# Performance work log

Hardware: AMD Instinct MI355X
Metric: run time of the kernel (lower is better)

## Reference

```python
import jax, jax.numpy as jnp
import numpy as np

B, N, NODE_IN, RAW_IN, COV, H = 4096, 128, 16, 128, 8, 64
BN_EPS = 1e-5


def setup_inputs() -> dict:
    key = jax.random.key(0)
    ks = jax.random.split(key, 24)
    rn = lambda k, s, sc=0.1: jax.random.normal(k, s, jnp.float32) * sc
    return {
        'x_str': jax.random.normal(ks[0], (B, N, NODE_IN), jnp.float32),
        'x_raw': jax.random.normal(ks[1], (B, RAW_IN), jnp.float32),
        'adj': jax.random.uniform(ks[2], (B, N, N), jnp.float32),
        'x_cov': jax.random.normal(ks[3], (B, COV), jnp.float32),
        'age': jax.random.uniform(ks[4], (B, 1), jnp.float32),
        'gc1_w': rn(ks[5], (NODE_IN, H)), 'gc1_b': jnp.zeros((H,), jnp.float32),
        'gc2_w': rn(ks[6], (H, H)), 'gc2_b': jnp.zeros((H,), jnp.float32),
        'bn_gamma': jnp.ones((N,), jnp.float32), 'bn_beta': jnp.zeros((N,), jnp.float32),
        'bn_mean': jnp.zeros((N,), jnp.float32), 'bn_var': jnp.ones((N,), jnp.float32),
        'attn_w': rn(ks[7], (H, 1)), 'attn_b': jnp.zeros((1,), jnp.float32),
        'na_w': rn(ks[8], (H, 1)), 'na_b': jnp.zeros((1,), jnp.float32),
        'beta_w1': rn(ks[9], (RAW_IN + COV + H, 64)), 'beta_b1': jnp.zeros((64,), jnp.float32),
        'beta_w2': rn(ks[10], (64, 1)), 'beta_b2': jnp.zeros((1,), jnp.float32),
        'af_w1': rn(ks[11], (H + RAW_IN, 32)), 'af_b1': jnp.zeros((32,), jnp.float32),
        'af_w2': rn(ks[12], (32, 1)), 'af_b2': jnp.zeros((1,), jnp.float32),
    }


def _gcn(x, adj, w, b):
    # A_hat = A + I; support = D^{-1/2} A_hat D^{-1/2} (diag matmuls as broadcasts)
    a_hat = adj + jnp.eye(N, dtype=adj.dtype)
    d_inv = jnp.sum(a_hat, axis=2) ** -0.5  # [B,N]
    d_inv = jnp.where(jnp.isinf(d_inv), 0.0, d_inv)
    support = d_inv[:, :, None] * a_hat * d_inv[:, None, :]  # [B,N,N]
    agg = jnp.einsum('bnm,bmf->bnf', support, x)
    return agg @ w + b


def reference(x_str, x_raw, adj, x_cov, age,
              gc1_w, gc1_b, gc2_w, gc2_b,
              bn_gamma, bn_beta, bn_mean, bn_var,
              attn_w, attn_b, na_w, na_b,
              beta_w1, beta_b1, beta_w2, beta_b2,
              af_w1, af_b1, af_w2, af_b2):
    h = jax.nn.elu(_gcn(x_str, adj, gc1_w, gc1_b))      # dropout = identity (eval)
    h = jax.nn.elu(_gcn(h, adj, gc2_w, gc2_b))
    # BatchNorm1d over channel dim N (eval mode, running stats)
    h = (h - bn_mean[None, :, None]) * jax.lax.rsqrt(bn_var + BN_EPS)[None, :, None]
    h = h * bn_gamma[None, :, None] + bn_beta[None, :, None]

    attn_scores = h @ attn_w + attn_b                   # [B,N,1]
    weights = jax.nn.softmax(attn_scores, axis=1)
    alpha_node = jax.nn.softplus(h @ na_w + na_b)       # [B,N,1]
    graph_emb = jnp.sum(h * weights, axis=1)            # [B,H]

    beta_in = jnp.concatenate([x_raw, x_cov, graph_emb], axis=1)
    beta = jax.nn.sigmoid(jnp.tanh(beta_in @ beta_w1 + beta_b1) @ beta_w2 + beta_b2)

    alpha_in = jnp.concatenate([graph_emb, x_raw], axis=1)
    decay_rate = jax.nn.softplus(jax.nn.relu(alpha_in @ af_w1 + af_b1) @ af_w2 + af_b2)

    pred = beta * (1.0 - decay_rate * age)
    return (pred, beta, decay_rate, alpha_node[..., 0], weights[..., 0])
```

## Files before the change

kernel.cpp:

```cpp
#include <hip/hip_runtime.h>
#include <hip/hip_bf16.h>
#include <math.h>

#define BB 4096
#define NN 128

typedef __attribute__((ext_vector_type(8))) __bf16 bf16x8;
typedef __attribute__((ext_vector_type(4))) __bf16 bf16x4;
typedef __attribute__((ext_vector_type(4))) float f32x4;

constexpr int OFF_XT   = 0;
constexpr int OFF_W1T  = 4352;
constexpr int OFF_AG1  = 9472;
constexpr int OFF_W2T  = 0;
constexpr int OFF_GEP  = 0;
constexpr int OFF_GP   = 8192;
constexpr int OFF_AP   = 9216;
constexpr int OFF_H1T  = 19712;
constexpr int OFF_AG2  = 19712;
constexpr int OFF_BNS  = 38144;
constexpr int OFF_BNB  = 38656;
constexpr int OFF_AW   = 39168;
constexpr int OFF_NW   = 39424;
constexpr int OFF_SCV  = 39680;
constexpr int OFF_GEV  = 40192;
constexpr int OFF_SCAL = 40448;
constexpr int SMEM_BYTES = 40464;

__device__ inline float eluf(float x)      { return x > 0.f ? x : __expf(x) - 1.f; }
__device__ inline float softplusf(float x) { return (x > 20.f) ? x : log1pf(__expf(x)); }

__global__ __launch_bounds__(512, 8)
void agp_kernel(const float* __restrict__ x_str, const float* __restrict__ x_raw,
                const float* __restrict__ adj,   const float* __restrict__ x_cov,
                const float* __restrict__ age,
                const float* __restrict__ gc1_w, const float* __restrict__ gc1_b,
                const float* __restrict__ gc2_w, const float* __restrict__ gc2_b,
                const float* __restrict__ bn_gamma, const float* __restrict__ bn_beta,
                const float* __restrict__ bn_mean,  const float* __restrict__ bn_var,
                const float* __restrict__ attn_w, const float* __restrict__ attn_b,
                const float* __restrict__ na_w,   const float* __restrict__ na_b,
                const float* __restrict__ beta_w1, const float* __restrict__ beta_b1,
                const float* __restrict__ beta_w2, const float* __restrict__ beta_b2,
                const float* __restrict__ af_w1,  const float* __restrict__ af_b1,
                const float* __restrict__ af_w2,  const float* __restrict__ af_b2,
                float* __restrict__ out)
{
    extern __shared__ __align__(16) char smraw[];
    __bf16* XT  = (__bf16*)(smraw + OFF_XT);
    __bf16* W1T = (__bf16*)(smraw + OFF_W1T);
    __bf16* AG1 = (__bf16*)(smraw + OFF_AG1);
    __bf16* W2T = (__bf16*)(smraw + OFF_W2T);
    __bf16* H1T = (__bf16*)(smraw + OFF_H1T);
    float* GEp  = (float*)(smraw + OFF_GEP);
    float* GP   = (float*)(smraw + OFF_GP);
    float* AP   = (float*)(smraw + OFF_AP);
    float* BNS  = (float*)(smraw + OFF_BNS);
    float* BNB  = (float*)(smraw + OFF_BNB);
    float* AW   = (float*)(smraw + OFF_AW);
    float* NWv  = (float*)(smraw + OFF_NW);
    float* SCv  = (float*)(smraw + OFF_SCV);
    float* GEv  = (float*)(smraw + OFF_GEV);
    float* SCAL = (float*)(smraw + OFF_SCAL);

    const int b = blockIdx.x;
    const int t = threadIdx.x;
    const int w    = t >> 6;
    const int lane = t & 63;
    const int ll = lane & 15;
    const int lh = lane >> 4;
    const int myrow = 16*w + ll;
    __bf16* AG2w = (__bf16*)(smraw + OFF_AG2) + w*1152;

    bf16x8 sf[4];
    float rs = 0.f;
    {
        const float* arow = adj + (size_t)b*NN*NN + (size_t)myrow*NN;
        const bool hasd = (((myrow >> 3) & 3) == lh);
        const int  dkt  = myrow >> 5;
        const int  didx = myrow & 7;
        #pragma unroll
        for (int kt = 0; kt < 4; ++kt) {
            int c0 = kt*32 + 8*lh;
            float4 a  = *reinterpret_cast<const float4*>(arow + c0);
            float4 a2 = *reinterpret_cast<const float4*>(arow + c0 + 4);
            if (kt == dkt && hasd) {
                a.x  += (didx==0)?1.f:0.f; a.y  += (didx==1)?1.f:0.f;
                a.z  += (didx==2)?1.f:0.f; a.w  += (didx==3)?1.f:0.f;
                a2.x += (didx==4)?1.f:0.f; a2.y += (didx==5)?1.f:0.f;
                a2.z += (didx==6)?1.f:0.f; a2.w += (didx==7)?1.f:0.f;
            }
            rs += ((a.x+a.y)+(a.z+a.w)) + ((a2.x+a2.y)+(a2.z+a2.w));
            bf16x8 s;
            s[0]=(__bf16)a.x;  s[1]=(__bf16)a.y;  s[2]=(__bf16)a.z;  s[3]=(__bf16)a.w;
            s[4]=(__bf16)a2.x; s[5]=(__bf16)a2.y; s[6]=(__bf16)a2.z; s[7]=(__bf16)a2.w;
            sf[kt] = s;
        }
        rs += __shfl_xor(rs, 16);
        rs += __shfl_xor(rs, 32);
    }
    {
        float dm = rsqrtf(rs);
        float4 xr = *reinterpret_cast<const float4*>(x_str + (size_t)b*NN*16 + myrow*16 + 4*lh);
        XT[(4*lh+0)*136 + myrow] = (__bf16)(xr.x * dm);
        XT[(4*lh+1)*136 + myrow] = (__bf16)(xr.y * dm);
        XT[(4*lh+2)*136 + myrow] = (__bf16)(xr.z * dm);
        XT[(4*lh+3)*136 + myrow] = (__bf16)(xr.w * dm);
    }
    if (t < 256) {
        int j = t & 63, k0 = (t >> 6) * 4;
        bf16x4 pk;
        pk[0] = (__bf16)gc1_w[(k0+0)*64 + j];
        pk[1] = (__bf16)gc1_w[(k0+1)*64 + j];
        pk[2] = (__bf16)gc1_w[(k0+2)*64 + j];
        pk[3] = (__bf16)gc1_w[(k0+3)*64 + j];
        *reinterpret_cast<bf16x4*>(&W1T[j*40 + k0]) = pk;
        bf16x4 z4; z4[0]=z4[1]=z4[2]=z4[3]=(__bf16)0.f;
        *reinterpret_cast<bf16x4*>(&W1T[(t>>2)*40 + 16 + (t&3)*4]) = z4;
    }
    {
        bf16x4 z4; z4[0]=z4[1]=z4[2]=z4[3]=(__bf16)0.f;
        *reinterpret_cast<bf16x4*>(&AG1[(t>>2)*40 + 16 + (t&3)*4]) = z4;
    }
    if (t < 128) {
        float g = bn_gamma[t], be = bn_beta[t], mu = bn_mean[t], va = bn_var[t];
        float sc = g * rsqrtf(va + 1e-5f);
        BNS[t] = sc;
        BNB[t] = be - mu*sc;
    } else if (t < 192) {
        AW[t-128] = attn_w[t-128];
    } else if (t < 256) {
        NWv[t-192] = na_w[t-192];
    }
    __syncthreads();

    float dr[4];
    #pragma unroll
    for (int r = 0; r < 4; ++r) dr[r] = rsqrtf(__shfl(rs, 4*lh + r));
    {
        f32x4 acc = {0.f, 0.f, 0.f, 0.f};
        #pragma unroll
        for (int kt = 0; kt < 4; ++kt) {
            bf16x8 bf = *reinterpret_cast<const bf16x8*>(&XT[ll*136 + kt*32 + 8*lh]);
            acc = __builtin_amdgcn_mfma_f32_16x16x32_bf16(sf[kt], bf, acc, 0, 0, 0);
        }
        #pragma unroll
        for (int r = 0; r < 4; ++r)
            AG1[(16*w + 4*lh + r)*40 + ll] = (__bf16)(acc[r] * dr[r]);
    }

    {
        bf16x8 a = *reinterpret_cast<const bf16x8*>(&AG1[(16*w + ll)*40 + 8*lh]);
        #pragma unroll
        for (int jt = 0; jt < 4; ++jt) {
            bf16x8 bf = *reinterpret_cast<const bf16x8*>(&W1T[(16*jt + ll)*40 + 8*lh]);
            f32x4 z = {0.f, 0.f, 0.f, 0.f};
            f32x4 acc = __builtin_amdgcn_mfma_f32_16x16x32_bf16(a, bf, z, 0, 0, 0);
            float bj = gc1_b[16*jt + ll];
            bf16x4 pk;
            #pragma unroll
            for (int r = 0; r < 4; ++r)
                pk[r] = (__bf16)(eluf(acc[r] + bj) * dr[r]);
            *reinterpret_cast<bf16x4*>(&H1T[(16*jt + ll)*136 + 16*w + 4*lh]) = pk;
        }
    }
    __syncthreads();

    float w2r[8];
    {
        int j = t & 63, k0 = (t >> 6) * 8;
        #pragma unroll
        for (int i = 0; i < 8; ++i) w2r[i] = gc2_w[(k0 + i)*64 + j];
    }

    bf16x4 pk2[4];
    {
        f32x4 acc2[4];
        #pragma unroll
        for (int jt = 0; jt < 4; ++jt) acc2[jt] = (f32x4){0.f, 0.f, 0.f, 0.f};
        #pragma unroll
        for (int kt = 0; kt < 4; ++kt) {
            #pragma unroll
            for (int jt = 0; jt < 4; ++jt) {
                bf16x8 bf = *reinterpret_cast<const bf16x8*>(&H1T[(16*jt + ll)*136 + kt*32 + 8*lh]);
                acc2[jt] = __builtin_amdgcn_mfma_f32_16x16x32_bf16(sf[kt], bf, acc2[jt], 0, 0, 0);
            }
        }
        #pragma unroll
        for (int jt = 0; jt < 4; ++jt)
            #pragma unroll
            for (int r = 0; r < 4; ++r)
                pk2[jt][r] = (__bf16)(acc2[jt][r] * dr[r]);
    }
    {
        int j = t & 63, k0 = (t >> 6) * 8;
        bf16x8 pv;
        #pragma unroll
        for (int i = 0; i < 8; ++i) pv[i] = (__bf16)w2r[i];
        *reinterpret_cast<bf16x8*>(&W2T[j*72 + k0]) = pv;
    }
    __syncthreads();

    #pragma unroll
    for (int jt = 0; jt < 4; ++jt)
        #pragma unroll
        for (int r = 0; r < 4; ++r)
            AG2w[(4*lh + r)*72 + 16*jt + ll] = pk2[jt][r];

    f32x4 hv[4];
    {
        #pragma unroll
        for (int jt = 0; jt < 4; ++jt) hv[jt] = (f32x4){0.f, 0.f, 0.f, 0.f};
        #pragma unroll
        for (int kt = 0; kt < 2; ++kt) {
            bf16x8 a = *reinterpret_cast<const bf16x8*>(&AG2w[ll*72 + kt*32 + 8*lh]);
            #pragma unroll
            for (int jt = 0; jt < 4; ++jt) {
                bf16x8 bf = *reinterpret_cast<const bf16x8*>(&W2T[(16*jt + ll)*72 + kt*32 + 8*lh]);
                hv[jt] = __builtin_amdgcn_mfma_f32_16x16x32_bf16(a, bf, hv[jt], 0, 0, 0);
            }
        }
        #pragma unroll
        for (int jt = 0; jt < 4; ++jt) {
            float bj = gc2_b[16*jt + ll];
            #pragma unroll
            for (int r = 0; r < 4; ++r) {
                int row = 16*w + 4*lh + r;
                hv[jt][r] = eluf(hv[jt][r] + bj) * BNS[row] + BNB[row];
            }
        }
    }

    float scA[4];
    {
        float aA[4] = {0,0,0,0}, aN[4] = {0,0,0,0};
        #pragma unroll
        for (int jt = 0; jt < 4; ++jt) {
            float wA = AW[16*jt + ll], wN = NWv[16*jt + ll];
            #pragma unroll
            for (int r = 0; r < 4; ++r) {
                aA[r] += hv[jt][r] * wA;
                aN[r] += hv[jt][r] * wN;
            }
        }
        #pragma unroll
        for (int m = 1; m <= 8; m <<= 1) {
            #pragma unroll
            for (int r = 0; r < 4; ++r) {
                aA[r] += __shfl_xor(aA[r], m);
                aN[r] += __shfl_xor(aN[r], m);
            }
        }
        float sA = attn_b[0], sN = na_b[0];
        #pragma unroll
        for (int r = 0; r < 4; ++r) scA[r] = aA[r] + sA;
        if (ll == 0) {
            #pragma unroll
            for (int r = 0; r < 4; ++r) {
                int row = 16*w + 4*lh + r;
                SCv[row] = scA[r];
                out[12288 + (size_t)b*NN + row] = softplusf(aN[r] + sN);
            }
        }
    }
    __syncthreads();

    {
        float s0 = SCv[lane], s1 = SCv[64 + lane];
        float mx = fmaxf(s0, s1);
        #pragma unroll
        for (int m = 32; m >= 1; m >>= 1) mx = fmaxf(mx, __shfl_xor(mx, m));
        float e0 = __expf(s0 - mx), e1 = __expf(s1 - mx);
        float sum = e0 + e1;
        #pragma unroll
        for (int m = 32; m >= 1; m >>= 1) sum += __shfl_xor(sum, m);
        float inv = 1.f / sum;
        float wt[4];
        #pragma unroll
        for (int r = 0; r < 4; ++r) wt[r] = __expf(scA[r] - mx) * inv;
        if (ll == 0) {
            #pragma unroll
            for (int r = 0; r < 4; ++r)
                out[536576 + (size_t)b*NN + 16*w + 4*lh + r] = wt[r];
        }
        #pragma unroll
        for (int jt = 0; jt < 4; ++jt) {
            float g = 0.f;
            #pragma unroll
            for (int r = 0; r < 4; ++r) g += hv[jt][r] * wt[r];
            GEp[(4*w + lh)*64 + 16*jt + ll] = g;
        }
    }
    __syncthreads();

    if (t < 64) {
        float ge = 0.f;
        #pragma unroll
        for (int g = 0; g < 32; ++g) ge += GEp[g*64 + t];
        GEv[t] = ge;
    }
    __syncthreads();

    if (t < 256) {
        int c = t >> 6, j = t & 63;
        float p = 0.f;
        for (int i = c*50; i < c*50 + 50; ++i) {
            float v = (i < 128) ? x_raw[(size_t)b*128 + i]
                    : (i < 136) ? x_cov[(size_t)b*8 + (i - 128)]
                                : GEv[i - 136];
            p += v * beta_w1[i*64 + j];
        }
        GP[c*64 + j] = p;
    } else if (t < 384) {
        int u = t - 256, c = u >> 5, j = u & 31;
        float p = 0.f;
        for (int i = c*48; i < c*48 + 48; ++i) {
            float v = (i < 64) ? GEv[i] : x_raw[(size_t)b*128 + (i - 64)];
            p += v * af_w1[i*32 + j];
        }
        AP[c*32 + j] = p;
    }
    __syncthreads();

    if (t < 64) {
        float acc = beta_b1[t] + GP[t] + GP[64 + t] + GP[128 + t] + GP[192 + t];
        float p = tanhf(acc) * beta_w2[t];
        #pragma unroll
        for (int m = 32; m >= 1; m >>= 1) p += __shfl_xor(p, m);
        if (t == 0) SCAL[0] = 1.f / (1.f + __expf(-(p + beta_b2[0])));
    } else if (t < 96) {
        int u = t - 64;
        float acc = af_b1[u] + AP[u] + AP[32 + u] + AP[64 + u] + AP[96 + u];
        float p = fmaxf(acc, 0.f) * af_w2[u];
        #pragma unroll
        for (int m = 16; m >= 1; m >>= 1) p += __shfl_xor(p, m);
        if (u == 0) SCAL[1] = softplusf(p + af_b2[0]);
    }
    __syncthreads();

    if (t == 0) {
        float bet = SCAL[0], dec = SCAL[1];
        out[b]        = bet * (1.f - dec * age[b]);
        out[4096 + b] = bet;
        out[8192 + b] = dec;
    }
}

extern "C" void kernel_launch(void* const* d_in, const int* in_sizes, int n_in,
                              void* d_out, int out_size, void* d_ws, size_t ws_size,
                              hipStream_t stream) {
    (void)in_sizes; (void)n_in; (void)out_size; (void)d_ws; (void)ws_size;
    const float* x_str   = (const float*)d_in[0];
    const float* x_raw   = (const float*)d_in[1];
    const float* adj     = (const float*)d_in[2];
    const float* x_cov   = (const float*)d_in[3];
    const float* age     = (const float*)d_in[4];
    const float* gc1_w   = (const float*)d_in[5];
    const float* gc1_b   = (const float*)d_in[6];
    const float* gc2_w   = (const float*)d_in[7];
    const float* gc2_b   = (const float*)d_in[8];
    const float* bn_g    = (const float*)d_in[9];
    const float* bn_b    = (const float*)d_in[10];
    const float* bn_m    = (const float*)d_in[11];
    const float* bn_v    = (const float*)d_in[12];
    const float* attn_w  = (const float*)d_in[13];
    const float* attn_b  = (const float*)d_in[14];
    const float* na_w    = (const float*)d_in[15];
    const float* na_b    = (const float*)d_in[16];
    const float* beta_w1 = (const float*)d_in[17];
    const float* beta_b1 = (const float*)d_in[18];
    const float* beta_w2 = (const float*)d_in[19];
    const float* beta_b2 = (const float*)d_in[20];
    const float* af_w1   = (const float*)d_in[21];
    const float* af_b1   = (const float*)d_in[22];
    const float* af_w2   = (const float*)d_in[23];
    const float* af_b2   = (const float*)d_in[24];
    float* out = (float*)d_out;

    (void)hipFuncSetAttribute((const void*)agp_kernel,
                              hipFuncAttributeMaxDynamicSharedMemorySize, SMEM_BYTES);
    agp_kernel<<<BB, 512, SMEM_BYTES, stream>>>(
        x_str, x_raw, adj, x_cov, age,
        gc1_w, gc1_b, gc2_w, gc2_b,
        bn_g, bn_b, bn_m, bn_v,
        attn_w, attn_b, na_w, na_b,
        beta_w1, beta_b1, beta_w2, beta_b2,
        af_w1, af_b1, af_w2, af_b2,
        out);
}
```

Baseline: 123.0 us.

## Use MFMA for adjacency row sums and spread tail MLPs across all threads

Adjacency row sums (degrees) are now computed with an MFMA against a ones vector instead of scalar adds and shuffles, and the results are redistributed to each lane by shuffles. Graph-embedding partials are reduced within each wave by shuffles before going to shared memory, which cuts the cross-wave sum from 32 to 8 entries. The beta and alpha MLP first layers are split across all 512 threads with shorter unrolled chunks, and the per-row output stores are vectorised to float4. These changes target the serial tail of the block. In exchange the row sum is now taken from bf16-rounded values, and the lane shuffling adds complexity.

```diff
diff --git a/kernel.cpp b/kernel.cpp
--- a/kernel.cpp
+++ b/kernel.cpp
@@ -14,8 +14,8 @@
 constexpr int OFF_AG1  = 9472;
 constexpr int OFF_W2T  = 0;
 constexpr int OFF_GEP  = 0;
-constexpr int OFF_GP   = 8192;
-constexpr int OFF_AP   = 9216;
+constexpr int OFF_GP   = 2048;
+constexpr int OFF_AP   = 4096;
 constexpr int OFF_H1T  = 19712;
 constexpr int OFF_AG2  = 19712;
 constexpr int OFF_BNS  = 38144;
@@ -73,7 +73,8 @@
     __bf16* AG2w = (__bf16*)(smraw + OFF_AG2) + w*1152;
 
     bf16x8 sf[4];
-    float rs = 0.f;
+    float dr[4];
+    float dm;
     {
         const float* arow = adj + (size_t)b*NN*NN + (size_t)myrow*NN;
         const bool hasd = (((myrow >> 3) & 3) == lh);
@@ -90,17 +91,28 @@
                 a2.x += (didx==4)?1.f:0.f; a2.y += (didx==5)?1.f:0.f;
                 a2.z += (didx==6)?1.f:0.f; a2.w += (didx==7)?1.f:0.f;
             }
-            rs += ((a.x+a.y)+(a.z+a.w)) + ((a2.x+a2.y)+(a2.z+a2.w));
             bf16x8 s;
             s[0]=(__bf16)a.x;  s[1]=(__bf16)a.y;  s[2]=(__bf16)a.z;  s[3]=(__bf16)a.w;
             s[4]=(__bf16)a2.x; s[5]=(__bf16)a2.y; s[6]=(__bf16)a2.z; s[7]=(__bf16)a2.w;
             sf[kt] = s;
         }
-        rs += __shfl_xor(rs, 16);
-        rs += __shfl_xor(rs, 32);
-    }
-    {
-        float dm = rsqrtf(rs);
+        bf16x8 ones;
+        #pragma unroll
+        for (int i = 0; i < 8; ++i) ones[i] = (__bf16)1.0f;
+        f32x4 rsacc = {0.f, 0.f, 0.f, 0.f};
+        #pragma unroll
+        for (int kt = 0; kt < 4; ++kt)
+            rsacc = __builtin_amdgcn_mfma_f32_16x16x32_bf16(sf[kt], ones, rsacc, 0, 0, 0);
+        #pragma unroll
+        for (int r = 0; r < 4; ++r) dr[r] = rsqrtf(__shfl(rsacc[r], 16*lh));
+        float tmp[4];
+        #pragma unroll
+        for (int r = 0; r < 4; ++r) tmp[r] = __shfl(rsacc[r], 16*(ll >> 2));
+        float s01 = (ll & 1) ? tmp[1] : tmp[0];
+        float s23 = (ll & 1) ? tmp[3] : tmp[2];
+        dm = rsqrtf((ll & 2) ? s23 : s01);
+    }
+    {
         float4 xr = *reinterpret_cast<const float4*>(x_str + (size_t)b*NN*16 + myrow*16 + 4*lh);
         XT[(4*lh+0)*136 + myrow] = (__bf16)(xr.x * dm);
         XT[(4*lh+1)*136 + myrow] = (__bf16)(xr.y * dm);
@@ -134,9 +146,6 @@
     }
     __syncthreads();
 
-    float dr[4];
-    #pragma unroll
-    for (int r = 0; r < 4; ++r) dr[r] = rsqrtf(__shfl(rs, 4*lh + r));
     {
         f32x4 acc = {0.f, 0.f, 0.f, 0.f};
         #pragma unroll
@@ -255,12 +264,12 @@
         #pragma unroll
         for (int r = 0; r < 4; ++r) scA[r] = aA[r] + sA;
         if (ll == 0) {
-            #pragma unroll
-            for (int r = 0; r < 4; ++r) {
-                int row = 16*w + 4*lh + r;
-                SCv[row] = scA[r];
-                out[12288 + (size_t)b*NN + row] = softplusf(aN[r] + sN);
-            }
+            float4 an4;
+            an4.x = softplusf(aN[0] + sN); an4.y = softplusf(aN[1] + sN);
+            an4.z = softplusf(aN[2] + sN); an4.w = softplusf(aN[3] + sN);
+            #pragma unroll
+            for (int r = 0; r < 4; ++r) SCv[16*w + 4*lh + r] = scA[r];
+            *reinterpret_cast<float4*>(&out[12288 + (size_t)b*NN + 16*w + 4*lh]) = an4;
         }
     }
     __syncthreads();
@@ -279,58 +288,92 @@
         #pragma unroll
         for (int r = 0; r < 4; ++r) wt[r] = __expf(scA[r] - mx) * inv;
         if (ll == 0) {
-            #pragma unroll
-            for (int r = 0; r < 4; ++r)
-                out[536576 + (size_t)b*NN + 16*w + 4*lh + r] = wt[r];
-        }
+            float4 w4; w4.x = wt[0]; w4.y = wt[1]; w4.z = wt[2]; w4.w = wt[3];
+            *reinterpret_cast<float4*>(&out[536576 + (size_t)b*NN + 16*w + 4*lh]) = w4;
+        }
+        float gg[4];
         #pragma unroll
         for (int jt = 0; jt < 4; ++jt) {
             float g = 0.f;
             #pragma unroll
             for (int r = 0; r < 4; ++r) g += hv[jt][r] * wt[r];
-            GEp[(4*w + lh)*64 + 16*jt + ll] = g;
-        }
+            g += __shfl_xor(g, 16);
+            g += __shfl_xor(g, 32);
+            gg[jt] = g;
+        }
+        float s01 = (lh & 1) ? gg[1] : gg[0];
+        float s23 = (lh & 1) ? gg[3] : gg[2];
+        GEp[w*64 + lane] = (lh & 2) ? s23 : s01;
     }
     __syncthreads();
 
     if (t < 64) {
         float ge = 0.f;
         #pragma unroll
-        for (int g = 0; g < 32; ++g) ge += GEp[g*64 + t];
+        for (int g = 0; g < 8; ++g) ge += GEp[g*64 + t];
         GEv[t] = ge;
     }
     __syncthreads();
 
-    if (t < 256) {
-        int c = t >> 6, j = t & 63;
+    {
+        const float* xr = x_raw + (size_t)b*128;
+        int j = t & 63;
         float p = 0.f;
-        for (int i = c*50; i < c*50 + 50; ++i) {
-            float v = (i < 128) ? x_raw[(size_t)b*128 + i]
-                    : (i < 136) ? x_cov[(size_t)b*8 + (i - 128)]
-                                : GEv[i - 136];
-            p += v * beta_w1[i*64 + j];
-        }
-        GP[c*64 + j] = p;
-    } else if (t < 384) {
-        int u = t - 256, c = u >> 5, j = u & 31;
-        float p = 0.f;
-        for (int i = c*48; i < c*48 + 48; ++i) {
-            float v = (i < 64) ? GEv[i] : x_raw[(size_t)b*128 + (i - 64)];
-            p += v * af_w1[i*32 + j];
-        }
-        AP[c*32 + j] = p;
+        if (w < 5) {
+            const float* bw = beta_w1 + (size_t)(w*25)*64 + j;
+            const float* xx = xr + w*25;
+            #pragma unroll
+            for (int k = 0; k < 25; ++k) p += xx[k] * bw[k*64];
+        } else if (w == 5) {
+            const float* cv = x_cov + (size_t)b*8;
+            #pragma unroll
+            for (int k = 0; k < 3; ++k)  p += xr[125+k] * beta_w1[(125+k)*64 + j];
+            #pragma unroll
+            for (int k = 0; k < 8; ++k)  p += cv[k]     * beta_w1[(128+k)*64 + j];
+            #pragma unroll
+            for (int k = 0; k < 14; ++k) p += GEv[k]    * beta_w1[(136+k)*64 + j];
+        } else if (w == 6) {
+            #pragma unroll
+            for (int k = 0; k < 25; ++k) p += GEv[14+k] * beta_w1[(150+k)*64 + j];
+        } else {
+            #pragma unroll
+            for (int k = 0; k < 25; ++k) p += GEv[39+k] * beta_w1[(175+k)*64 + j];
+        }
+        GP[w*64 + j] = p;
+
+        int j2 = t & 31, ch = t >> 5;
+        float q = 0.f;
+        if (ch < 5) {
+            int i0 = ch*12;
+            #pragma unroll
+            for (int k = 0; k < 12; ++k) q += GEv[i0+k] * af_w1[(i0+k)*32 + j2];
+        } else if (ch == 5) {
+            #pragma unroll
+            for (int k = 0; k < 4; ++k) q += GEv[60+k] * af_w1[(60+k)*32 + j2];
+            #pragma unroll
+            for (int k = 0; k < 8; ++k) q += xr[k]     * af_w1[(64+k)*32 + j2];
+        } else {
+            int i0 = ch*12 - 64;
+            #pragma unroll
+            for (int k = 0; k < 12; ++k) q += xr[i0+k] * af_w1[(i0+k+64)*32 + j2];
+        }
+        AP[ch*32 + j2] = q;
     }
     __syncthreads();
 
     if (t < 64) {
-        float acc = beta_b1[t] + GP[t] + GP[64 + t] + GP[128 + t] + GP[192 + t];
+        float acc = beta_b1[t];
+        #pragma unroll
+        for (int c = 0; c < 8; ++c) acc += GP[c*64 + t];
         float p = tanhf(acc) * beta_w2[t];
         #pragma unroll
         for (int m = 32; m >= 1; m >>= 1) p += __shfl_xor(p, m);
         if (t == 0) SCAL[0] = 1.f / (1.f + __expf(-(p + beta_b2[0])));
     } else if (t < 96) {
         int u = t - 64;
-        float acc = af_b1[u] + AP[u] + AP[32 + u] + AP[64 + u] + AP[96 + u];
+        float acc = af_b1[u];
+        #pragma unroll
+        for (int c = 0; c < 16; ++c) acc += AP[c*32 + u];
         float p = fmaxf(acc, 0.f) * af_w2[u];
         #pragma unroll
         for (int m = 16; m >= 1; m >>= 1) p += __shfl_xor(p, m);
```

Measured after the change: 104.4 us, median of 2. 15.2% less time.
